# Performance work log

Measured on AMD Instinct MI355X. Metric: run time of the kernel, lower is better.

Reference implementation:

```python
import jax, jax.numpy as jnp
import numpy as np

B, H, W, F_HEX, F_GLB = 2, 48, 48, 150, 7
D, NH, L, DF, M = 512, 8, 4, 2048, 128
MAX_W, MAX_H, ATK, REC = 48, 48, 8, 20
S = H * W
DK = D // NH


def _ln(x, g, b):
    m = jnp.mean(x, -1, keepdims=True)
    v = jnp.mean(jnp.square(x - m), -1, keepdims=True)
    return (x - m) * jax.lax.rsqrt(v + 1e-5) * g + b


def _mha(q, k, v, wq, bq, wk, bk, wv, bv, wo, bo, mask=None):
    Bq, Sq, _ = q.shape
    Sk = k.shape[1]
    Q = (q @ wq + bq).reshape(Bq, Sq, NH, DK)
    K = (k @ wk + bk).reshape(Bq, Sk, NH, DK)
    V = (v @ wv + bv).reshape(Bq, Sk, NH, DK)
    s = jnp.einsum('bqhd,bkhd->bhqk', Q, K) / np.float32(np.sqrt(DK))
    if mask is not None:
        s = jnp.where(mask == 0, jnp.float32(-1e9), s)
    a = jax.nn.softmax(s, -1)
    o = jnp.einsum('bhqk,bkhd->bqhd', a, V).reshape(Bq, Sq, D)
    return o @ wo + bo


def setup_inputs():
    key = jax.random.key(0)
    ks = iter(jax.random.split(key, 64))
    w = lambda *sh: jax.random.normal(next(ks), sh, jnp.float32) * 0.02
    z = lambda *sh: jnp.zeros(sh, jnp.float32)
    o = lambda *sh: jnp.ones(sh, jnp.float32)
    return dict(
        map_representation=jax.random.normal(next(ks), (B, H, W, F_HEX), jnp.float32),
        global_features=jax.random.normal(next(ks), (B, F_GLB), jnp.float32),
        memory=jax.random.normal(next(ks), (B, M, D), jnp.float32),
        fog_mask=jax.random.randint(next(ks), (B, H, W), 0, 2, jnp.int32),
        hex_w=w(F_HEX, D), hex_b=z(D), glob_w=w(F_GLB, D), glob_b=z(D),
        mem_wq=w(D, D), mem_bq=z(D), mem_wk=w(D, D), mem_bk=z(D),
        mem_wv=w(D, D), mem_bv=z(D), mem_wo=w(D, D), mem_bo=z(D),
        gate_w=w(2 * D, D), gate_b=z(D),
        mn1_g=o(D), mn1_b=z(D), mn2_g=o(D), mn2_b=z(D),
        lw_q=w(L, D, D), lb_q=z(L, D), lw_k=w(L, D, D), lb_k=z(L, D),
        lw_v=w(L, D, D), lb_v=z(L, D), lw_o=w(L, D, D), lb_o=z(L, D),
        ln1_g=o(L, D), ln1_b=z(L, D), ln2_g=o(L, D), ln2_b=z(L, D),
        ff1_w=w(L, D, DF), ff1_b=z(L, DF), ff2_w=w(L, DF, D), ff2_b=z(L, D),
        pool_w=w(D, 1), pool_b=z(1),
        sx_w=w(D, MAX_W), sx_b=z(MAX_W), sy_w=w(D, MAX_H), sy_b=z(MAX_H),
        tx_w=w(D, MAX_W), tx_b=z(MAX_W), ty_w=w(D, MAX_H), ty_b=z(MAX_H),
        atk_w=w(D, ATK), atk_b=z(ATK), rec_w=w(D, REC), rec_b=z(REC),
        et_w=w(D, 1), et_b=z(1), val_w=w(D, 1), val_b=z(1),
    )


def reference(map_representation, global_features, memory, fog_mask,
              hex_w, hex_b, glob_w, glob_b,
              mem_wq, mem_bq, mem_wk, mem_bk, mem_wv, mem_bv, mem_wo, mem_bo,
              gate_w, gate_b, mn1_g, mn1_b, mn2_g, mn2_b,
              lw_q, lb_q, lw_k, lb_k, lw_v, lb_v, lw_o, lb_o,
              ln1_g, ln1_b, ln2_g, ln2_b, ff1_w, ff1_b, ff2_w, ff2_b,
              pool_w, pool_b, sx_w, sx_b, sy_w, sy_b, tx_w, tx_b, ty_w, ty_b,
              atk_w, atk_b, rec_w, rec_b, et_w, et_b, val_w, val_b):
    # project hex + global features, flatten map to token sequence [B,S,D]
    hexf = map_representation @ hex_w + hex_b
    glob = global_features @ glob_w + glob_b
    seq = (hexf + glob[:, None, None, :]).reshape(B, S, D)
    am = fog_mask.reshape(B, S)[:, None, None, :]  # key mask [B,1,1,S]

    # memory module: cross-attn conditioning + gated memory update (shared MHA weights)
    mem_out = _mha(seq, memory, memory, mem_wq, mem_bq, mem_wk, mem_bk, mem_wv, mem_bv, mem_wo, mem_bo)
    x = _ln(seq + mem_out, mn1_g, mn1_b)
    mem_upd = _mha(memory, seq, seq, mem_wq, mem_bq, mem_wk, mem_bk, mem_wv, mem_bv, mem_wo, mem_bo)
    gate = jax.nn.sigmoid(jnp.concatenate([memory, mem_upd], -1) @ gate_w + gate_b)
    new_memory = _ln(gate * mem_upd + (1.0 - gate) * memory, mn2_g, mn2_b)

    def block(xc, p):
        wq, bq, wk, bk, wv, bv, wo, bo, g1, b1, g2, b2, f1w, f1b, f2w, f2b = p
        att = _mha(xc, xc, xc, wq, bq, wk, bk, wv, bv, wo, bo, mask=am)
        xc = _ln(xc + att, g1, b1)
        h = jax.nn.gelu(xc @ f1w + f1b, approximate=False) @ f2w + f2b
        return _ln(xc + h, g2, b2), None

    x, _ = jax.lax.scan(block, x, (lw_q, lb_q, lw_k, lb_k, lw_v, lb_v, lw_o, lb_o,
                                   ln1_g, ln1_b, ln2_g, ln2_b, ff1_w, ff1_b, ff2_w, ff2_b))

    # attention pooling over tokens
    pw = jax.nn.softmax((x @ pool_w + pool_b)[..., 0], -1)  # [B,S]
    pooled = jnp.einsum('bs,bsd->bd', pw, x)

    return (pooled @ sx_w + sx_b, pooled @ sy_w + sy_b,
            pooled @ tx_w + tx_b, pooled @ ty_w + ty_b,
            pooled @ atk_w + atk_b, pooled @ rec_w + rec_b,
            pooled @ et_w + et_b, pooled @ val_w + val_b, new_memory)
```

## Files before the change

### kernel.cpp

```cpp
#include <hip/hip_runtime.h>
#include <hip/hip_bf16.h>

typedef __hip_bfloat16 bf16;
typedef unsigned short u16;
typedef __attribute__((ext_vector_type(8))) short short8;
typedef __attribute__((ext_vector_type(4))) float f32x4;

__device__ inline float b2f(u16 u){ unsigned int x = ((unsigned int)u) << 16; float f; __builtin_memcpy(&f, &x, 4); return f; }
__device__ inline u16 f2bits(float f){ __hip_bfloat16 h = __float2bfloat16(f); u16 u; __builtin_memcpy(&u, &h, 2); return u; }
__device__ inline void unpk(unsigned int w, float& a, float& b){ a = b2f((u16)(w & 0xffffu)); b = b2f((u16)(w >> 16)); }

__device__ __forceinline__ unsigned int pkbf(float a, float b)
{
  unsigned int ua = __float_as_uint(a) + 0x8000u;
  unsigned int ub = __float_as_uint(b) + 0x8000u;
  return __builtin_amdgcn_perm(ub, ua, 0x07060302u);
}

__global__ __launch_bounds__(512) void detect_k(const unsigned int* __restrict__ raw, int* __restrict__ flag)
{
  __shared__ int cnt;
  if (threadIdx.x == 0) cnt = 0;
  __syncthreads();
  unsigned int w = raw[threadIdx.x];
  unsigned int b = w & 0x7fffu;
  int pat = (b >= 0x2000u && b <= 0x4400u) ? 1 : 0;
#pragma unroll
  for (int o = 32; o; o >>= 1) pat += __shfl_xor(pat, o);
  if ((threadIdx.x & 63) == 0) atomicAdd(&cnt, pat);
  __syncthreads();
  if (threadIdx.x == 0) flag[0] = (cnt > 320) ? 1 : 0;
}

struct CvtArgs { const void* p[55]; int off[56]; int sz[55]; };

__global__ __launch_bounds__(256) void cvtall8_k(CvtArgs a, bf16* __restrict__ dst,
                                                 const int* __restrict__ flag)
{
  int g8 = blockIdx.x * 256 + threadIdx.x;
  int gid = g8 * 8;
  if (gid >= a.off[55]) return;
  int lo = 0, hi = 54;
  while (lo < hi) { int mid = (lo + hi + 1) >> 1; if (gid >= a.off[mid]) lo = mid; else hi = mid - 1; }
  int t = lo, i = gid - a.off[t];
  int n = a.sz[t];
  uint4 ov;
  if (flag[0]) {
    const u16* src = (const u16*)a.p[t];
    if (i + 8 <= n) {
      ov = *(const uint4*)(src + i);
    } else {
      u16 tmp[8];
#pragma unroll
      for (int j = 0; j < 8; j++) tmp[j] = (i + j < n) ? src[i + j] : (u16)0;
      __builtin_memcpy(&ov, tmp, 16);
    }
  } else {
    const float* src = (const float*)a.p[t];
    float v[8];
    if (i + 8 <= n) {
      uint4 f0 = *(const uint4*)(src + i);
      uint4 f1 = *(const uint4*)(src + i + 4);
      __builtin_memcpy(&v[0], &f0, 16);
      __builtin_memcpy(&v[4], &f1, 16);
    } else {
#pragma unroll
      for (int j = 0; j < 8; j++) v[j] = (i + j < n) ? src[i + j] : 0.f;
    }
    u16 o8[8];
#pragma unroll
    for (int j = 0; j < 8; j++) o8[j] = f2bits(v[j]);
    __builtin_memcpy(&ov, o8, 16);
  }
  *(uint4*)((u16*)dst + gid) = ov;
}

__global__ __launch_bounds__(256) void gemm_k(
    const bf16* __restrict__ A, int lda, long long sAb, long long sAh,
    const bf16* __restrict__ B, int ldb, long long sBb, long long sBh,
    bf16* __restrict__ C, int ldc, long long sCb, long long sCh,
    int M, int N, int K, int HZ,
    const bf16* __restrict__ bias,
    const bf16* __restrict__ res, int ldres,
    const float* __restrict__ extra, int extraDiv,
    float alpha, int mode)
{
  __shared__ u16 As[64][40];
  __shared__ u16 Bs[64][40];
  int z = blockIdx.z;
  int bz = z / HZ, hz = z - bz * HZ;
  A += (size_t)bz * sAb + (size_t)hz * sAh;
  B += (size_t)bz * sBb + (size_t)hz * sBh;
  C += (size_t)bz * sCb + (size_t)hz * sCh;

  int m0 = blockIdx.y * 64, n0 = blockIdx.x * 64;
  int t = threadIdx.x;
  int r = t >> 2, c0 = (t & 3) << 3;
  int lane = t & 63, wv = t >> 6, lr = lane & 15, lq = lane >> 4;

  f32x4 acc[4];
#pragma unroll
  for (int i = 0; i < 4; i++) acc[i] = (f32x4){0.f, 0.f, 0.f, 0.f};

  const u16* Ag = (const u16*)A;
  const u16* Bg = (const u16*)B;
  bool aok = (m0 + r < M), bok = (n0 + r < N);
  const u16* arow = Ag + (size_t)(m0 + r) * lda + c0;
  const u16* brow = Bg + (size_t)(n0 + r) * ldb + c0;

  uint4 av = {0u,0u,0u,0u}, bv = {0u,0u,0u,0u};
  if (aok) av = *(const uint4*)(arow);
  if (bok) bv = *(const uint4*)(brow);

  for (int kt = 0; kt < K; kt += 32) {
    __syncthreads();
    *(uint4*)&As[r][c0] = av;
    *(uint4*)&Bs[r][c0] = bv;
    uint4 av2 = {0u,0u,0u,0u}, bv2 = {0u,0u,0u,0u};
    int nk = kt + 32;
    if (nk < K) {
      if (aok) av2 = *(const uint4*)(arow + nk);
      if (bok) bv2 = *(const uint4*)(brow + nk);
    }
    __syncthreads();
    short8 af = *(const short8*)&As[wv * 16 + lr][lq * 8];
#pragma unroll
    for (int nt = 0; nt < 4; nt++) {
      short8 bfr = *(const short8*)&Bs[nt * 16 + lr][lq * 8];
      acc[nt] = __builtin_amdgcn_mfma_f32_16x16x32_bf16(af, bfr, acc[nt], 0, 0, 0);
    }
    av = av2; bv = bv2;
  }

#pragma unroll
  for (int nt = 0; nt < 4; nt++) {
    int nn = n0 + nt * 16 + lr;
    if (nn >= N) continue;
    float bb = bias ? (float)bias[nn] : 0.f;
#pragma unroll
    for (int rr = 0; rr < 4; rr++) {
      int mm = m0 + wv * 16 + lq * 4 + rr;
      if (mm >= M) continue;
      float v = acc[nt][rr] * alpha + bb;
      if (mode == 1)      v += extra[(mm / extraDiv) * 512 + nn];
      else if (mode == 2) v = 0.5f * v * (1.f + erff(v * 0.70710678118654752f));
      else if (mode == 4) v += (float)res[(size_t)mm * ldres + nn];
      else if (mode == 5) v = 1.f / (1.f + expf(-v));
      C[(size_t)mm * ldc + nn] = __float2bfloat16(v);
    }
  }
}

__device__ __forceinline__ int swz(int row, int cg)
{
  return row * 64 + ((cg ^ (row & 3) ^ (((row >> 3) & 1) << 2)) << 3);
}

__global__ __launch_bounds__(256) void flash_k(
    const bf16* __restrict__ Qp, long long sQb,
    const bf16* __restrict__ Kp, long long sKb,
    const bf16* __restrict__ VTp, long long sVz,
    float* __restrict__ oAcc, long long sOb,
    float* __restrict__ lAcc, int Ml,
    const int* __restrict__ fog,
    int tilesPerSplit, int SkLen)
{
  __shared__ u16 Kl[64 * 64];
  __shared__ u16 Vl[64 * 64];
  __shared__ u16 fgl16[2304];

  const float SC = 0.125f * 1.44269504088896340736f;
  int z = blockIdx.y, b = z >> 3, h = z & 7;
  int qt = blockIdx.x;
  int kt0 = blockIdx.z * tilesPerSplit;
  int t = threadIdx.x, lane = t & 63, w = t >> 6;
  int lr = lane & 15, lq = lane >> 4;
  int useMask = (fog != nullptr);

  const u16* Qg = (const u16*)Qp + (size_t)b * sQb + h * 64;
  const u16* Kg = (const u16*)Kp + (size_t)b * sKb + h * 64;
  const u16* Vg = (const u16*)VTp + (size_t)z * sVz;

  if (useMask) {
    for (int j = t; j < SkLen; j += 256) fgl16[j] = fog[b * 2304 + j] ? 0xFFFFu : 0u;
  }

  int qrow = qt * 64 + w * 16 + lr;
  short8 qf0, qf1;
  {
    union { short8 s; u16 u[8]; } i0, i1, o0, o1;
    i0.s = *(const short8*)(Qg + (size_t)qrow * 512 + lq * 8);
    i1.s = *(const short8*)(Qg + (size_t)qrow * 512 + 32 + lq * 8);
#pragma unroll
    for (int j = 0; j < 8; j++) {
      o0.u[j] = f2bits(b2f(i0.u[j]) * SC);
      o1.u[j] = f2bits(b2f(i1.u[j]) * SC);
    }
    qf0 = o0.s; qf1 = o1.s;
  }

  short8 ones8;
  {
    union { short8 s; u16 u[8]; } on;
#pragma unroll
    for (int j = 0; j < 8; j++) on.u[j] = 0x3F80u;
    ones8 = on.s;
  }

  int rowA[4], kAd0[4], kAd1[4];
#pragma unroll
  for (int nt = 0; nt < 4; nt++) {
    rowA[nt] = 32 * (nt >> 1) + 8 * (lr >> 2) + 4 * (nt & 1) + (lr & 3);
    kAd0[nt] = swz(rowA[nt], lq);
    kAd1[nt] = swz(rowA[nt], lq + 4);
  }
  int vAd0[4], vAd1[4];
#pragma unroll
  for (int dt = 0; dt < 4; dt++) {
    vAd0[dt] = swz(dt * 16 + lr, lq);
    vAd1[dt] = swz(dt * 16 + lr, lq + 4);
  }

  f32x4 o[4], ol;
#pragma unroll
  for (int i = 0; i < 4; i++) o[i] = (f32x4){0.f, 0.f, 0.f, 0.f};
  ol = (f32x4){0.f, 0.f, 0.f, 0.f};

  int rr = t >> 2, cg = t & 3, cs = cg * 8;
  int wAd0 = swz(rr, cg), wAd1 = swz(rr, cg + 4);

  const u16* krow = Kg + (size_t)(kt0 * 64 + rr) * 512 + cs;
  const u16* vrow = Vg + (size_t)rr * SkLen + kt0 * 64 + cs;
  uint4 ka = *(const uint4*)(krow);
  uint4 kb = *(const uint4*)(krow + 32);
  uint4 va = *(const uint4*)(vrow);
  uint4 vb = *(const uint4*)(vrow + 32);

  for (int kti = 0; kti < tilesPerSplit; kti++) {
    int kt = kt0 + kti;
    __syncthreads();
    *(uint4*)&Kl[wAd0] = ka;
    *(uint4*)&Kl[wAd1] = kb;
    *(uint4*)&Vl[wAd0] = va;
    *(uint4*)&Vl[wAd1] = vb;
    if (kti + 1 < tilesPerSplit) {
      krow += 64 * 512;
      vrow += 64;
      ka = *(const uint4*)(krow);
      kb = *(const uint4*)(krow + 32);
      va = *(const uint4*)(vrow);
      vb = *(const uint4*)(vrow + 32);
    }
    __syncthreads();

    f32x4 s[4];
#pragma unroll
    for (int nt = 0; nt < 4; nt++) {
      s[nt] = (f32x4){0.f, 0.f, 0.f, 0.f};
      short8 kf0 = *(const short8*)&Kl[kAd0[nt]];
      short8 kf1 = *(const short8*)&Kl[kAd1[nt]];
      s[nt] = __builtin_amdgcn_mfma_f32_16x16x32_bf16(kf0, qf0, s[nt], 0, 0, 0);
      s[nt] = __builtin_amdgcn_mfma_f32_16x16x32_bf16(kf1, qf1, s[nt], 0, 0, 0);
    }

    union { unsigned int u[4]; short8 s8; } pk0, pk1;
#pragma unroll
    for (int nt = 0; nt < 4; nt++) {
      float p0 = exp2f(s[nt][0]), p1 = exp2f(s[nt][1]);
      float p2 = exp2f(s[nt][2]), p3 = exp2f(s[nt][3]);
      unsigned int w0 = pkbf(p0, p1);
      unsigned int w1 = pkbf(p2, p3);
      if (useMask) {
        int key = kt * 64 + 32 * (nt >> 1) + 8 * lq + 4 * (nt & 1);
        uint2 mm = *(const uint2*)&fgl16[key];
        w0 &= mm.x; w1 &= mm.y;
      }
      if (nt < 2) { pk0.u[(nt & 1) * 2] = w0; pk0.u[(nt & 1) * 2 + 1] = w1; }
      else        { pk1.u[(nt & 1) * 2] = w0; pk1.u[(nt & 1) * 2 + 1] = w1; }
    }
#pragma unroll
    for (int dt = 0; dt < 4; dt++) {
      short8 vf0 = *(const short8*)&Vl[vAd0[dt]];
      short8 vf1 = *(const short8*)&Vl[vAd1[dt]];
      o[dt] = __builtin_amdgcn_mfma_f32_16x16x32_bf16(pk0.s8, vf0, o[dt], 0, 0, 0);
      o[dt] = __builtin_amdgcn_mfma_f32_16x16x32_bf16(pk1.s8, vf1, o[dt], 0, 0, 0);
    }
    ol = __builtin_amdgcn_mfma_f32_16x16x32_bf16(pk0.s8, ones8, ol, 0, 0, 0);
    ol = __builtin_amdgcn_mfma_f32_16x16x32_bf16(pk1.s8, ones8, ol, 0, 0, 0);
  }

  if (lr == 0) {
#pragma unroll
    for (int r2 = 0; r2 < 4; r2++)
      atomicAdd(&lAcc[z * Ml + qt * 64 + w * 16 + lq * 4 + r2], ol[r2]);
  }

  float* ob = oAcc + (size_t)b * sOb;
  int qb = qt * 64 + w * 16 + lq * 4;
#pragma unroll
  for (int dt = 0; dt < 4; dt++)
#pragma unroll
    for (int r2 = 0; r2 < 4; r2++)
      atomicAdd(&ob[(size_t)(qb + r2) * 512 + h * 64 + dt * 16 + lr], o[dt][r2]);
}

__global__ __launch_bounds__(256) void fdiv4_k(const float* __restrict__ oAcc,
                                               const float* __restrict__ lAcc,
                                               int Mq, int Ml, int rows,
                                               bf16* __restrict__ out)
{
  int i = (blockIdx.x * 256 + threadIdx.x) * 4;
  if (i >= rows * 512) return;
  int row = i >> 9, col = i & 511;
  int b = row / Mq, q = row - b * Mq;
  int zz = b * 8 + (col >> 6);
  float l = lAcc[zz * Ml + q];
  float inv = (l > 0.f) ? 1.f / l : 0.f;
  float4 v = *(const float4*)(oAcc + i);
  u16 o4[4] = {f2bits(v.x * inv), f2bits(v.y * inv), f2bits(v.z * inv), f2bits(v.w * inv)};
  unsigned int lo = o4[0] | ((unsigned)o4[1] << 16);
  unsigned int hi = o4[2] | ((unsigned)o4[3] << 16);
  *(uint2*)((u16*)out + i) = (uint2){lo, hi};
}

__global__ __launch_bounds__(256) void transpose_k(const bf16* __restrict__ in, bf16* __restrict__ out,
                                                   int R, int C, int Rpad, long long inB, long long outB)
{
  __shared__ u16 tile[32][33];
  const u16* ip = (const u16*)in + (size_t)blockIdx.z * inB;
  u16* op = (u16*)out + (size_t)blockIdx.z * outB;
  int c0 = blockIdx.x * 32, r0 = blockIdx.y * 32;
  int tx = threadIdx.x & 31, ty = threadIdx.x >> 5;
#pragma unroll
  for (int j = 0; j < 4; j++) {
    int rr = r0 + ty + j * 8, cc = c0 + tx;
    u16 v = 0;
    if (rr < R && cc < C) v = ip[(size_t)rr * C + cc];
    tile[ty + j * 8][tx] = v;
  }
  __syncthreads();
#pragma unroll
  for (int j = 0; j < 4; j++) {
    int oc = c0 + ty + j * 8;
    if (oc < C && r0 + tx < Rpad) op[(size_t)oc * Rpad + r0 + tx] = tile[tx][ty + j * 8];
  }
}

__global__ __launch_bounds__(256) void headT_k(const bf16* __restrict__ in, bf16* __restrict__ out,
                                               int Sk, int rowbase, int bstride)
{
  __shared__ u16 tile[32][33];
  int z = blockIdx.z, b = z >> 3, h = z & 7;
  const u16* ip = (const u16*)in + ((size_t)(rowbase + b * bstride)) * 512 + h * 64;
  u16* op = (u16*)out + (size_t)z * 64 * Sk;
  int r0 = blockIdx.x * 32, c0 = blockIdx.y * 32;
  int tx = threadIdx.x & 31, ty = threadIdx.x >> 5;
#pragma unroll
  for (int j = 0; j < 4; j++)
    tile[ty + j * 8][tx] = ip[(size_t)(r0 + ty + j * 8) * 512 + c0 + tx];
  __syncthreads();
#pragma unroll
  for (int j = 0; j < 4; j++)
    op[(size_t)(c0 + ty + j * 8) * Sk + r0 + tx] = tile[tx][ty + j * 8];
}

__global__ __launch_bounds__(256) void ln_k(const bf16* __restrict__ in, const bf16* __restrict__ g,
                                            const bf16* __restrict__ bb, bf16* __restrict__ out)
{
  size_t row = blockIdx.x * 4 + (threadIdx.x >> 6);
  int lane = threadIdx.x & 63;
  const u16* ip = (const u16*)in + row * 512 + lane * 8;
  uint4 rv = *(const uint4*)ip;
  float v[8];
  unpk(rv.x, v[0], v[1]); unpk(rv.y, v[2], v[3]); unpk(rv.z, v[4], v[5]); unpk(rv.w, v[6], v[7]);
  float s = 0.f, s2 = 0.f;
#pragma unroll
  for (int k = 0; k < 8; k++) { s += v[k]; s2 += v[k] * v[k]; }
#pragma unroll
  for (int o = 32; o; o >>= 1) { s += __shfl_xor(s, o); s2 += __shfl_xor(s2, o); }
  float mean = s * (1.f / 512.f);
  float var = s2 * (1.f / 512.f) - mean * mean;
  float rstd = rsqrtf(var + 1e-5f);
  uint4 gv = *(const uint4*)((const u16*)g + lane * 8);
  uint4 bv = *(const uint4*)((const u16*)bb + lane * 8);
  float gf[8], bf2[8];
  unpk(gv.x, gf[0], gf[1]); unpk(gv.y, gf[2], gf[3]); unpk(gv.z, gf[4], gf[5]); unpk(gv.w, gf[6], gf[7]);
  unpk(bv.x, bf2[0], bf2[1]); unpk(bv.y, bf2[2], bf2[3]); unpk(bv.z, bf2[4], bf2[5]); unpk(bv.w, bf2[6], bf2[7]);
  u16 o8[8];
#pragma unroll
  for (int k = 0; k < 8; k++) o8[k] = f2bits((v[k] - mean) * rstd * gf[k] + bf2[k]);
  uint4 ov;
  ov.x = o8[0] | ((unsigned)o8[1] << 16); ov.y = o8[2] | ((unsigned)o8[3] << 16);
  ov.z = o8[4] | ((unsigned)o8[5] << 16); ov.w = o8[6] | ((unsigned)o8[7] << 16);
  *(uint4*)((u16*)out + row * 512 + lane * 8) = ov;
}

__global__ void glob_k(const bf16* __restrict__ gf, const bf16* __restrict__ gw,
                       const bf16* __restrict__ gb, float* __restrict__ out)
{
  int i = blockIdx.x * 256 + threadIdx.x; if (i >= 1024) return;
  int b = i >> 9, d = i & 511;
  float s = (float)gb[d];
#pragma unroll
  for (int f = 0; f < 7; f++) s += (float)gf[b * 7 + f] * (float)gw[f * 512 + d];
  out[i] = s;
}

__global__ void padA_k(const bf16* __restrict__ in, bf16* __restrict__ out)
{
  int i = blockIdx.x * 256 + threadIdx.x; if (i >= 4608 * 160) return;
  int r = i / 160, c = i - r * 160;
  out[i] = (c < 150) ? in[r * 150 + c] : __float2bfloat16(0.f);
}

__global__ void catg_k(const bf16* __restrict__ mem, const bf16* __restrict__ mu, bf16* __restrict__ out)
{
  int i = blockIdx.x * 256 + threadIdx.x; if (i >= 256 * 1024) return;
  int r = i >> 10, c = i & 1023;
  out[i] = (c < 512) ? mem[r * 512 + c] : mu[r * 512 + c - 512];
}

__global__ void gcomb_k(const bf16* __restrict__ g, const bf16* __restrict__ mu,
                        const bf16* __restrict__ mem, bf16* __restrict__ out)
{
  int i = blockIdx.x * 256 + threadIdx.x; if (i >= 131072) return;
  float gg = (float)g[i];
  out[i] = __float2bfloat16(gg * (float)mu[i] + (1.f - gg) * (float)mem[i]);
}

__global__ __launch_bounds__(64) void plog_k(const bf16* __restrict__ x, const bf16* __restrict__ pw,
                                             const bf16* __restrict__ pb, float* __restrict__ out)
{
  size_t row = blockIdx.x; int lane = threadIdx.x;
  uint4 xv = *(const uint4*)((const u16*)x + row * 512 + lane * 8);
  uint4 wv = *(const uint4*)((const u16*)pw + lane * 8);
  float v[8], w[8];
  unpk(xv.x, v[0], v[1]); unpk(xv.y, v[2], v[3]); unpk(xv.z, v[4], v[5]); unpk(xv.w, v[6], v[7]);
  unpk(wv.x, w[0], w[1]); unpk(wv.y, w[2], w[3]); unpk(wv.z, w[4], w[5]); unpk(wv.w, w[6], w[7]);
  float s = 0.f;
#pragma unroll
  for (int k = 0; k < 8; k++) s += v[k] * w[k];
#pragma unroll
  for (int o = 32; o; o >>= 1) s += __shfl_xor(s, o);
  if (lane == 0) out[row] = s + (float)pb[0];
}

__global__ __launch_bounds__(256) void psm_k(const float* __restrict__ lg, float* __restrict__ pw)
{
  __shared__ float red[4];
  int b = blockIdx.x, tid = threadIdx.x;
  const float* p = lg + b * 2304;
  float vals[9]; float mx = -3e38f;
#pragma unroll
  for (int i = 0; i < 9; i++) {
    int j = tid + i * 256;
    float x = (j < 2304) ? p[j] : -3e38f;
    vals[i] = x; mx = fmaxf(mx, x);
  }
#pragma unroll
  for (int o = 32; o; o >>= 1) mx = fmaxf(mx, __shfl_xor(mx, o));
  if ((tid & 63) == 0) red[tid >> 6] = mx;
  __syncthreads();
  mx = fmaxf(fmaxf(red[0], red[1]), fmaxf(red[2], red[3]));
  float sum = 0.f;
#pragma unroll
  for (int i = 0; i < 9; i++) {
    int j = tid + i * 256;
    if (j < 2304) { float e = expf(vals[i] - mx); vals[i] = e; sum += e; }
  }
  __syncthreads();
#pragma unroll
  for (int o = 32; o; o >>= 1) sum += __shfl_xor(sum, o);
  if ((tid & 63) == 0) red[tid >> 6] = sum;
  __syncthreads();
  sum = red[0] + red[1] + red[2] + red[3];
  float inv = 1.f / sum;
#pragma unroll
  for (int i = 0; i < 9; i++) {
    int j = tid + i * 256;
    if (j < 2304) pw[b * 2304 + j] = vals[i] * inv;
  }
}

__global__ __launch_bounds__(256) void pool1_k(const float* __restrict__ pw, const bf16* __restrict__ x,
                                               float* __restrict__ out)
{
  int b = blockIdx.y, chunk = blockIdx.x, t = threadIdx.x;
  float a0 = 0.f, a1 = 0.f;
  for (int s = 0; s < 64; s++) {
    int tok = chunk * 64 + s;
    float wv = pw[b * 2304 + tok];
    const u16* xp = (const u16*)x + ((size_t)(b * 2304 + tok)) * 512;
    a0 += wv * b2f(xp[t]);
    a1 += wv * b2f(xp[t + 256]);
  }
  atomicAdd(&out[b * 512 + t], a0);
  atomicAdd(&out[b * 512 + t + 256], a1);
}

__global__ void heads_k(const float* __restrict__ pooled,
                        const bf16* w0, const bf16* b0, const bf16* w1, const bf16* b1,
                        const bf16* w2, const bf16* b2, const bf16* w3, const bf16* b3,
                        const bf16* w4, const bf16* b4, const bf16* w5, const bf16* b5,
                        const bf16* w6, const bf16* b6, const bf16* w7, const bf16* b7,
                        void* __restrict__ outv, const int* __restrict__ flag)
{
  int idx = blockIdx.x * 256 + threadIdx.x; if (idx >= 444) return;
  const bf16* W[8] = {w0, w1, w2, w3, w4, w5, w6, w7};
  const bf16* Bi[8] = {b0, b1, b2, b3, b4, b5, b6, b7};
  int b = idx / 222, j = idx - b * 222;
  const int sizes[8]  = {48, 48, 48, 48, 8, 20, 1, 1};
  const int outoff[8] = {0, 96, 192, 288, 384, 400, 440, 442};
  int h = 0, basec = 0;
  while (h < 7 && j >= basec + sizes[h]) { basec += sizes[h]; ++h; }
  int col = j - basec;
  const bf16* wp = W[h]; int nc = sizes[h];
  float s = (float)Bi[h][col];
  for (int k = 0; k < 512; k++) s += pooled[b * 512 + k] * (float)wp[k * nc + col];
  int e = outoff[h] + b * nc + col;
  if (flag[0]) ((bf16*)outv)[e] = __float2bfloat16(s);
  else         ((float*)outv)[e] = s;
}

__global__ void outstore_k(const bf16* __restrict__ nm, void* __restrict__ outv,
                           const int* __restrict__ flag)
{
  int i = blockIdx.x * 256 + threadIdx.x; if (i >= 131072) return;
  if (flag[0]) ((bf16*)outv)[444 + i] = nm[i];
  else         ((float*)outv)[444 + i] = (float)nm[i];
}


static inline void gemm(hipStream_t st, const bf16* A, int lda, long long sAb, long long sAh,
                        const bf16* B, int ldb, long long sBb, long long sBh,
                        bf16* C, int ldc, long long sCb, long long sCh,
                        int M, int N, int K, int BZ, int HZ,
                        const bf16* bias, const bf16* res, int ldres,
                        const float* extra, int extraDiv, float alpha, int mode)
{
  dim3 g((N + 63) / 64, (M + 63) / 64, BZ * HZ);
  gemm_k<<<g, dim3(256), 0, st>>>(A, lda, sAb, sAh, B, ldb, sBb, sBh, C, ldc, sCb, sCh,
                                  M, N, K, HZ, bias, res, ldres, extra, extraDiv, alpha, mode);
}

static inline void transp(hipStream_t st, const bf16* in, bf16* out, int R, int C, int Rpad,
                          long long inB, long long outB, int Z)
{
  dim3 g((C + 31) / 32, (Rpad + 31) / 32, Z);
  transpose_k<<<g, dim3(256), 0, st>>>(in, out, R, C, Rpad, inB, outB);
}

extern "C" void kernel_launch(void* const* d_in, const int* in_sizes, int n_in,
                              void* d_out, int out_size, void* d_ws, size_t ws_size,
                              hipStream_t stream)
{
  (void)in_sizes; (void)n_in; (void)out_size;
  const int* fog = (const int*)d_in[3];

  static const int kSz[55] = {
    691200, 14, 131072, 76800, 512, 3584, 512,
    262144, 512, 262144, 512, 262144, 512, 262144, 512,
    524288, 512, 512, 512, 512, 512,
    1048576, 2048, 1048576, 2048, 1048576, 2048, 1048576, 2048,
    2048, 2048, 2048, 2048,
    4194304, 8192, 4194304, 2048,
    512, 1,
    24576, 48, 24576, 48, 24576, 48, 24576, 48,
    4096, 8, 10240, 20, 512, 1, 512, 1};
  static const int kIdx[55] = {
    0, 1, 2, 4, 5, 6, 7,
    8, 9, 10, 11, 12, 13, 14, 15,
    16, 17, 18, 19, 20, 21,
    22, 23, 24, 25, 26, 27, 28, 29,
    30, 31, 32, 33,
    34, 35, 36, 37,
    38, 39,
    40, 41, 42, 43, 44, 45, 46, 47,
    48, 49, 50, 51, 52, 53, 54, 55};

  CvtArgs ca;
  size_t cum[55]; int coffi = 0;
  for (int t = 0; t < 55; t++) {
    cum[t] = (size_t)coffi;
    ca.p[t] = d_in[kIdx[t]];
    ca.off[t] = coffi;
    ca.sz[t] = kSz[t];
    coffi += (kSz[t] + 7) & ~7;
  }
  ca.off[55] = coffi;
  size_t coff = (size_t)coffi;

  const int S = 2304, NROW = 4608, CATROW = 4864;
  const long long RS = (long long)S * 512;

  char* basep = (char*)d_ws; size_t off = 0;
  auto alloc = [&](size_t elems, size_t esz) -> void* {
    void* p = basep + off; off += (elems * esz + 255) & ~(size_t)255; return p;
  };

  bf16* canon = (bf16*)alloc(coff, 2);
  int* dflag = (int*)alloc(64, 4);
  bf16* tHex = (bf16*)alloc(512 * 160, 2);
  bf16* aPad = (bf16*)alloc((size_t)NROW * 160, 2);
  bf16* tWq = (bf16*)alloc(512 * 512, 2);
  bf16* tWk = (bf16*)alloc(512 * 512, 2);
  bf16* tWv = (bf16*)alloc(512 * 512, 2);
  bf16* tWo = (bf16*)alloc(512 * 512, 2);
  bf16* tGate = (bf16*)alloc(512 * 1024, 2);
  bf16* tLq = (bf16*)alloc(4 * 512 * 512, 2);
  bf16* tLk = (bf16*)alloc(4 * 512 * 512, 2);
  bf16* tLv = (bf16*)alloc(4 * 512 * 512, 2);
  bf16* tLo = (bf16*)alloc(4 * 512 * 512, 2);
  bf16* tF1 = (bf16*)alloc(4ULL * 2048 * 512, 2);
  bf16* tF2 = (bf16*)alloc(4ULL * 512 * 2048, 2);
  float* globF = (float*)alloc(1024, 4);
  bf16* catX = (bf16*)alloc((size_t)CATROW * 512, 2);
  bf16* Qc = (bf16*)alloc((size_t)CATROW * 512, 2);
  bf16* Kc = (bf16*)alloc((size_t)CATROW * 512, 2);
  bf16* Vc = (bf16*)alloc((size_t)CATROW * 512, 2);
  bf16* VmemT = (bf16*)alloc(16ULL * 64 * 128, 2);
  bf16* VsT = (bf16*)alloc(16ULL * 64 * S, 2);
  bf16* mo = (bf16*)alloc((size_t)NROW * 512, 2);
  bf16* tmp1 = (bf16*)alloc((size_t)NROW * 512, 2);
  bf16* xbuf = (bf16*)alloc((size_t)NROW * 512, 2);
  bf16* x2buf = (bf16*)alloc((size_t)NROW * 512, 2);
  bf16* mu0 = (bf16*)alloc(256 * 512, 2);
  bf16* mup = (bf16*)alloc(256 * 512, 2);
  bf16* catg = (bf16*)alloc(256 * 1024, 2);
  bf16* gateb = (bf16*)alloc(256 * 512, 2);
  bf16* nmpre = (bf16*)alloc(256 * 512, 2);
  bf16* nmout = (bf16*)alloc(256 * 512, 2);
  float* plog = (float*)alloc(NROW, 4);
  float* pwv = (float*)alloc(NROW, 4);
  float* pooledF = (float*)alloc(1024, 4);
  float* oAcc = (float*)alloc((size_t)NROW * 512, 4);
  float* lAcc = (float*)alloc(16 * 2304, 4);
  bf16* hbuf = (bf16*)alloc((size_t)NROW * 2048, 2);
  if (off > ws_size) return;

  detect_k<<<1, 512, 0, stream>>>((const unsigned int*)d_in[0], dflag);
  cvtall8_k<<<(coffi / 8 + 255) / 256, 256, 0, stream>>>(ca, canon, dflag);

  auto T = [&](int t) -> const bf16* { return canon + cum[t]; };
  const bf16* map_rep = T(0);
  const bf16* gfeat   = T(1);
  const bf16* memin   = T(2);
  const bf16* hex_w = T(3);  const bf16* hex_b = T(4);
  const bf16* glob_w = T(5); const bf16* glob_b = T(6);
  const bf16* mem_wq = T(7);  const bf16* mem_bq = T(8);
  const bf16* mem_wk = T(9);  const bf16* mem_bk = T(10);
  const bf16* mem_wv = T(11); const bf16* mem_bv = T(12);
  const bf16* mem_wo = T(13); const bf16* mem_bo = T(14);
  const bf16* gate_w = T(15); const bf16* gate_b = T(16);
  const bf16* mn1_g = T(17); const bf16* mn1_b = T(18);
  const bf16* mn2_g = T(19); const bf16* mn2_b = T(20);
  const bf16* lw_q = T(21); const bf16* lb_q = T(22);
  const bf16* lw_k = T(23); const bf16* lb_k = T(24);
  const bf16* lw_v = T(25); const bf16* lb_v = T(26);
  const bf16* lw_o = T(27); const bf16* lb_o = T(28);
  const bf16* ln1_g = T(29); const bf16* ln1_b = T(30);
  const bf16* ln2_g = T(31); const bf16* ln2_b = T(32);
  const bf16* ff1_w = T(33); const bf16* ff1_b = T(34);
  const bf16* ff2_w = T(35); const bf16* ff2_b = T(36);
  const bf16* pool_w = T(37); const bf16* pool_b = T(38);

  transp(stream, hex_w, tHex, 150, 512, 160, 0, 0, 1);
  transp(stream, mem_wq, tWq, 512, 512, 512, 0, 0, 1);
  transp(stream, mem_wk, tWk, 512, 512, 512, 0, 0, 1);
  transp(stream, mem_wv, tWv, 512, 512, 512, 0, 0, 1);
  transp(stream, mem_wo, tWo, 512, 512, 512, 0, 0, 1);
  transp(stream, gate_w, tGate, 1024, 512, 1024, 0, 0, 1);
  transp(stream, lw_q, tLq, 512, 512, 512, 262144, 262144, 4);
  transp(stream, lw_k, tLk, 512, 512, 512, 262144, 262144, 4);
  transp(stream, lw_v, tLv, 512, 512, 512, 262144, 262144, 4);
  transp(stream, lw_o, tLo, 512, 512, 512, 262144, 262144, 4);
  transp(stream, ff1_w, tF1, 512, 2048, 512, 1048576, 1048576, 4);
  transp(stream, ff2_w, tF2, 2048, 512, 2048, 1048576, 1048576, 4);

  glob_k<<<4, 256, 0, stream>>>(gfeat, glob_w, glob_b, globF);
  padA_k<<<(NROW * 160 + 255) / 256, 256, 0, stream>>>(map_rep, aPad);
  gemm(stream, aPad, 160, 0, 0, tHex, 160, 0, 0, catX, 512, 0, 0,
       NROW, 512, 160, 1, 1, hex_b, nullptr, 0, globF, S, 1.f, 1);
  hipMemcpyAsync(catX + (size_t)NROW * 512, memin, 256 * 512 * 2, hipMemcpyDeviceToDevice, stream);

  gemm(stream, catX, 512, 0, 0, tWq, 512, 0, 0, Qc, 512, 0, 0, CATROW, 512, 512, 1, 1, mem_bq, nullptr, 0, nullptr, 1, 1.f, 0);
  gemm(stream, catX, 512, 0, 0, tWk, 512, 0, 0, Kc, 512, 0, 0, CATROW, 512, 512, 1, 1, mem_bk, nullptr, 0, nullptr, 1, 1.f, 0);
  gemm(stream, catX, 512, 0, 0, tWv, 512, 0, 0, Vc, 512, 0, 0, CATROW, 512, 512, 1, 1, mem_bv, nullptr, 0, nullptr, 1, 1.f, 0);

  headT_k<<<dim3(4, 2, 16), 256, 0, stream>>>(Vc, VmemT, 128, NROW, 128);
  hipMemsetAsync(oAcc, 0, (size_t)NROW * 512 * 4, stream);
  hipMemsetAsync(lAcc, 0, 16 * 2304 * 4, stream);
  flash_k<<<dim3(36, 16, 1), 256, 0, stream>>>(Qc, RS, Kc + (size_t)NROW * 512, 128 * 512,
                                               VmemT, 64 * 128, oAcc, RS, lAcc, 2304,
                                               nullptr, 2, 128);
  fdiv4_k<<<(NROW * 128 + 255) / 256, 256, 0, stream>>>(oAcc, lAcc, 2304, 2304, NROW, mo);
  gemm(stream, mo, 512, 0, 0, tWo, 512, 0, 0, tmp1, 512, 0, 0,
       NROW, 512, 512, 1, 1, mem_bo, catX, 512, nullptr, 1, 1.f, 4);
  ln_k<<<NROW / 4, 256, 0, stream>>>(tmp1, mn1_g, mn1_b, xbuf);

  headT_k<<<dim3(72, 2, 16), 256, 0, stream>>>(Vc, VsT, S, 0, S);
  hipMemsetAsync(oAcc, 0, 256 * 512 * 4, stream);
  hipMemsetAsync(lAcc, 0, 16 * 128 * 4, stream);
  flash_k<<<dim3(2, 16, 6), 256, 0, stream>>>(Qc + (size_t)NROW * 512, 128 * 512, Kc, RS,
                                              VsT, 64LL * S, oAcc, 128 * 512, lAcc, 128,
                                              nullptr, 6, S);
  fdiv4_k<<<(256 * 128 + 255) / 256, 256, 0, stream>>>(oAcc, lAcc, 128, 128, 256, mu0);
  gemm(stream, mu0, 512, 0, 0, tWo, 512, 0, 0, mup, 512, 0, 0,
       256, 512, 512, 1, 1, mem_bo, nullptr, 0, nullptr, 1, 1.f, 0);
  catg_k<<<(256 * 1024 + 255) / 256, 256, 0, stream>>>(memin, mup, catg);
  gemm(stream, catg, 1024, 0, 0, tGate, 1024, 0, 0, gateb, 512, 0, 0,
       256, 512, 1024, 1, 1, gate_b, nullptr, 0, nullptr, 1, 1.f, 5);
  gcomb_k<<<(131072 + 255) / 256, 256, 0, stream>>>(gateb, mup, memin, nmpre);
  ln_k<<<64, 256, 0, stream>>>(nmpre, mn2_g, mn2_b, nmout);
  outstore_k<<<(131072 + 255) / 256, 256, 0, stream>>>(nmout, d_out, dflag);

  for (int l = 0; l < 4; l++) {
    gemm(stream, xbuf, 512, 0, 0, tLq + (size_t)l * 262144, 512, 0, 0, Qc, 512, 0, 0,
         NROW, 512, 512, 1, 1, lb_q + l * 512, nullptr, 0, nullptr, 1, 1.f, 0);
    gemm(stream, xbuf, 512, 0, 0, tLk + (size_t)l * 262144, 512, 0, 0, Kc, 512, 0, 0,
         NROW, 512, 512, 1, 1, lb_k + l * 512, nullptr, 0, nullptr, 1, 1.f, 0);
    gemm(stream, xbuf, 512, 0, 0, tLv + (size_t)l * 262144, 512, 0, 0, Vc, 512, 0, 0,
         NROW, 512, 512, 1, 1, lb_v + l * 512, nullptr, 0, nullptr, 1, 1.f, 0);
    headT_k<<<dim3(72, 2, 16), 256, 0, stream>>>(Vc, VsT, S, 0, S);
    hipMemsetAsync(oAcc, 0, (size_t)NROW * 512 * 4, stream);
    hipMemsetAsync(lAcc, 0, 16 * 2304 * 4, stream);
    flash_k<<<dim3(36, 16, 2), 256, 0, stream>>>(Qc, RS, Kc, RS, VsT, 64LL * S,
                                                 oAcc, RS, lAcc, 2304, fog, 18, S);
    fdiv4_k<<<(NROW * 128 + 255) / 256, 256, 0, stream>>>(oAcc, lAcc, 2304, 2304, NROW, mo);
    gemm(stream, mo, 512, 0, 0, tLo + (size_t)l * 262144, 512, 0, 0, tmp1, 512, 0, 0,
         NROW, 512, 512, 1, 1, lb_o + l * 512, xbuf, 512, nullptr, 1, 1.f, 4);
    ln_k<<<NROW / 4, 256, 0, stream>>>(tmp1, ln1_g + l * 512, ln1_b + l * 512, x2buf);
    gemm(stream, x2buf, 512, 0, 0, tF1 + (size_t)l * 1048576, 512, 0, 0, hbuf, 2048, 0, 0,
         NROW, 2048, 512, 1, 1, ff1_b + l * 2048, nullptr, 0, nullptr, 1, 1.f, 2);
    gemm(stream, hbuf, 2048, 0, 0, tF2 + (size_t)l * 1048576, 2048, 0, 0, tmp1, 512, 0, 0,
         NROW, 512, 2048, 1, 1, ff2_b + l * 512, x2buf, 512, nullptr, 1, 1.f, 4);
    ln_k<<<NROW / 4, 256, 0, stream>>>(tmp1, ln2_g + l * 512, ln2_b + l * 512, xbuf);
  }

  plog_k<<<NROW, 64, 0, stream>>>(xbuf, pool_w, pool_b, plog);
  psm_k<<<2, 256, 0, stream>>>(plog, pwv);
  hipMemsetAsync(pooledF, 0, 1024 * sizeof(float), stream);
  pool1_k<<<dim3(36, 2), 256, 0, stream>>>(pwv, xbuf, pooledF);

  heads_k<<<2, 256, 0, stream>>>(pooledF,
      T(39), T(40), T(41), T(42), T(43), T(44), T(45), T(46),
      T(47), T(48), T(49), T(50), T(51), T(52), T(53), T(54),
      d_out, dflag);
}
```

Baseline: 1.184 ms.

## Fuse Q/K/V projections into one GEMM and retune attention split

Packs the Q, K and V weight matrices and biases into one concatenated [1536x512] operand, so each projection stage runs one GEMM writing an interleaved QKV buffer instead of three GEMMs. The flash and transpose kernels gain row-stride parameters to read from the interleaved buffer. The two memsets become one zeroing kernel. The self-attention key split goes from 2 to 3 chunks, and exp2f is replaced by the hardware exp2 builtin. The aim is fewer launches and better GEMM occupancy, at the cost of strided Q/K reads and more split-K partial accumulation.

```diff
diff --git a/kernel.cpp b/kernel.cpp
--- a/kernel.cpp
+++ b/kernel.cpp
@@ -157,8 +157,8 @@
 }
 
 __global__ __launch_bounds__(256) void flash_k(
-    const bf16* __restrict__ Qp, long long sQb,
-    const bf16* __restrict__ Kp, long long sKb,
+    const bf16* __restrict__ Qp, long long sQb, int sQr,
+    const bf16* __restrict__ Kp, long long sKb, int sKr,
     const bf16* __restrict__ VTp, long long sVz,
     float* __restrict__ oAcc, long long sOb,
     float* __restrict__ lAcc, int Ml,
@@ -189,8 +189,8 @@
   short8 qf0, qf1;
   {
     union { short8 s; u16 u[8]; } i0, i1, o0, o1;
-    i0.s = *(const short8*)(Qg + (size_t)qrow * 512 + lq * 8);
-    i1.s = *(const short8*)(Qg + (size_t)qrow * 512 + 32 + lq * 8);
+    i0.s = *(const short8*)(Qg + (size_t)qrow * sQr + lq * 8);
+    i1.s = *(const short8*)(Qg + (size_t)qrow * sQr + 32 + lq * 8);
 #pragma unroll
     for (int j = 0; j < 8; j++) {
       o0.u[j] = f2bits(b2f(i0.u[j]) * SC);
@@ -229,7 +229,7 @@
   int rr = t >> 2, cg = t & 3, cs = cg * 8;
   int wAd0 = swz(rr, cg), wAd1 = swz(rr, cg + 4);
 
-  const u16* krow = Kg + (size_t)(kt0 * 64 + rr) * 512 + cs;
+  const u16* krow = Kg + (size_t)(kt0 * 64 + rr) * sKr + cs;
   const u16* vrow = Vg + (size_t)rr * SkLen + kt0 * 64 + cs;
   uint4 ka = *(const uint4*)(krow);
   uint4 kb = *(const uint4*)(krow + 32);
@@ -244,7 +244,7 @@
     *(uint4*)&Vl[wAd0] = va;
     *(uint4*)&Vl[wAd1] = vb;
     if (kti + 1 < tilesPerSplit) {
-      krow += 64 * 512;
+      krow += (size_t)64 * sKr;
       vrow += 64;
       ka = *(const uint4*)(krow);
       kb = *(const uint4*)(krow + 32);
@@ -266,8 +266,10 @@
     union { unsigned int u[4]; short8 s8; } pk0, pk1;
 #pragma unroll
     for (int nt = 0; nt < 4; nt++) {
-      float p0 = exp2f(s[nt][0]), p1 = exp2f(s[nt][1]);
-      float p2 = exp2f(s[nt][2]), p3 = exp2f(s[nt][3]);
+      float p0 = __builtin_amdgcn_exp2f(s[nt][0]);
+      float p1 = __builtin_amdgcn_exp2f(s[nt][1]);
+      float p2 = __builtin_amdgcn_exp2f(s[nt][2]);
+      float p3 = __builtin_amdgcn_exp2f(s[nt][3]);
       unsigned int w0 = pkbf(p0, p1);
       unsigned int w1 = pkbf(p2, p3);
       if (useMask) {
@@ -323,6 +325,32 @@
   *(uint2*)((u16*)out + i) = (uint2){lo, hi};
 }
 
+__global__ __launch_bounds__(256) void zero2_k(float* __restrict__ p1, int n1,
+                                               float* __restrict__ p2, int n2)
+{
+  int i = blockIdx.x * 256 + threadIdx.x;
+  if (i < n1) p1[i] = 0.f;
+  if (i < n2) p2[i] = 0.f;
+}
+
+__global__ void biasfuse_k(const bf16* __restrict__ mbq, const bf16* __restrict__ mbk,
+                           const bf16* __restrict__ mbv, const bf16* __restrict__ lbq,
+                           const bf16* __restrict__ lbk, const bf16* __restrict__ lbv,
+                           bf16* __restrict__ out)
+{
+  int j = blockIdx.x * 256 + threadIdx.x;
+  if (j >= 5 * 1536) return;
+  int g = j / 1536, r = j - g * 1536;
+  int which = r >> 9, c = r & 511;
+  const bf16* src;
+  if (g == 0) src = (which == 0) ? mbq : (which == 1) ? mbk : mbv;
+  else {
+    const bf16* base = (which == 0) ? lbq : (which == 1) ? lbk : lbv;
+    src = base + (g - 1) * 512;
+  }
+  out[j] = src[c];
+}
+
 __global__ __launch_bounds__(256) void transpose_k(const bf16* __restrict__ in, bf16* __restrict__ out,
                                                    int R, int C, int Rpad, long long inB, long long outB)
 {
@@ -347,17 +375,17 @@
 }
 
 __global__ __launch_bounds__(256) void headT_k(const bf16* __restrict__ in, bf16* __restrict__ out,
-                                               int Sk, int rowbase, int bstride)
+                                               int Sk, int rowbase, int bstride, int instride)
 {
   __shared__ u16 tile[32][33];
   int z = blockIdx.z, b = z >> 3, h = z & 7;
-  const u16* ip = (const u16*)in + ((size_t)(rowbase + b * bstride)) * 512 + h * 64;
+  const u16* ip = (const u16*)in + ((size_t)(rowbase + b * bstride)) * instride + h * 64;
   u16* op = (u16*)out + (size_t)z * 64 * Sk;
   int r0 = blockIdx.x * 32, c0 = blockIdx.y * 32;
   int tx = threadIdx.x & 31, ty = threadIdx.x >> 5;
 #pragma unroll
   for (int j = 0; j < 4; j++)
-    tile[ty + j * 8][tx] = ip[(size_t)(r0 + ty + j * 8) * 512 + c0 + tx];
+    tile[ty + j * 8][tx] = ip[(size_t)(r0 + ty + j * 8) * instride + c0 + tx];
   __syncthreads();
 #pragma unroll
   for (int j = 0; j < 4; j++)
@@ -591,7 +619,8 @@
   size_t coff = (size_t)coffi;
 
   const int S = 2304, NROW = 4608, CATROW = 4864;
-  const long long RS = (long long)S * 512;
+  const long long QR = 1536;
+  const long long RSQ = (long long)S * QR;
 
   char* basep = (char*)d_ws; size_t off = 0;
   auto alloc = [&](size_t elems, size_t esz) -> void* {
@@ -602,22 +631,17 @@
   int* dflag = (int*)alloc(64, 4);
   bf16* tHex = (bf16*)alloc(512 * 160, 2);
   bf16* aPad = (bf16*)alloc((size_t)NROW * 160, 2);
-  bf16* tWq = (bf16*)alloc(512 * 512, 2);
-  bf16* tWk = (bf16*)alloc(512 * 512, 2);
-  bf16* tWv = (bf16*)alloc(512 * 512, 2);
+  bf16* tQKVmem = (bf16*)alloc(1536 * 512, 2);
   bf16* tWo = (bf16*)alloc(512 * 512, 2);
   bf16* tGate = (bf16*)alloc(512 * 1024, 2);
-  bf16* tLq = (bf16*)alloc(4 * 512 * 512, 2);
-  bf16* tLk = (bf16*)alloc(4 * 512 * 512, 2);
-  bf16* tLv = (bf16*)alloc(4 * 512 * 512, 2);
+  bf16* tLqkv = (bf16*)alloc(4ULL * 1536 * 512, 2);
   bf16* tLo = (bf16*)alloc(4 * 512 * 512, 2);
   bf16* tF1 = (bf16*)alloc(4ULL * 2048 * 512, 2);
   bf16* tF2 = (bf16*)alloc(4ULL * 512 * 2048, 2);
+  bf16* fbias = (bf16*)alloc(5 * 1536, 2);
   float* globF = (float*)alloc(1024, 4);
   bf16* catX = (bf16*)alloc((size_t)CATROW * 512, 2);
-  bf16* Qc = (bf16*)alloc((size_t)CATROW * 512, 2);
-  bf16* Kc = (bf16*)alloc((size_t)CATROW * 512, 2);
-  bf16* Vc = (bf16*)alloc((size_t)CATROW * 512, 2);
+  bf16* QKV = (bf16*)alloc((size_t)CATROW * 1536, 2);
   bf16* VmemT = (bf16*)alloc(16ULL * 64 * 128, 2);
   bf16* VsT = (bf16*)alloc(16ULL * 64 * S, 2);
   bf16* mo = (bf16*)alloc((size_t)NROW * 512, 2);
@@ -665,17 +689,19 @@
   const bf16* pool_w = T(37); const bf16* pool_b = T(38);
 
   transp(stream, hex_w, tHex, 150, 512, 160, 0, 0, 1);
-  transp(stream, mem_wq, tWq, 512, 512, 512, 0, 0, 1);
-  transp(stream, mem_wk, tWk, 512, 512, 512, 0, 0, 1);
-  transp(stream, mem_wv, tWv, 512, 512, 512, 0, 0, 1);
+  transp(stream, mem_wq, tQKVmem, 512, 512, 512, 0, 0, 1);
+  transp(stream, mem_wk, tQKVmem + 262144, 512, 512, 512, 0, 0, 1);
+  transp(stream, mem_wv, tQKVmem + 524288, 512, 512, 512, 0, 0, 1);
   transp(stream, mem_wo, tWo, 512, 512, 512, 0, 0, 1);
   transp(stream, gate_w, tGate, 1024, 512, 1024, 0, 0, 1);
-  transp(stream, lw_q, tLq, 512, 512, 512, 262144, 262144, 4);
-  transp(stream, lw_k, tLk, 512, 512, 512, 262144, 262144, 4);
-  transp(stream, lw_v, tLv, 512, 512, 512, 262144, 262144, 4);
+  transp(stream, lw_q, tLqkv, 512, 512, 512, 262144, 786432, 4);
+  transp(stream, lw_k, tLqkv + 262144, 512, 512, 512, 262144, 786432, 4);
+  transp(stream, lw_v, tLqkv + 524288, 512, 512, 512, 262144, 786432, 4);
   transp(stream, lw_o, tLo, 512, 512, 512, 262144, 262144, 4);
   transp(stream, ff1_w, tF1, 512, 2048, 512, 1048576, 1048576, 4);
   transp(stream, ff2_w, tF2, 2048, 512, 2048, 1048576, 1048576, 4);
+  biasfuse_k<<<(5 * 1536 + 255) / 256, 256, 0, stream>>>(mem_bq, mem_bk, mem_bv,
+                                                         lb_q, lb_k, lb_v, fbias);
 
   glob_k<<<4, 256, 0, stream>>>(gfeat, glob_w, glob_b, globF);
   padA_k<<<(NROW * 160 + 255) / 256, 256, 0, stream>>>(map_rep, aPad);
@@ -683,27 +709,24 @@
        NROW, 512, 160, 1, 1, hex_b, nullptr, 0, globF, S, 1.f, 1);
   hipMemcpyAsync(catX + (size_t)NROW * 512, memin, 256 * 512 * 2, hipMemcpyDeviceToDevice, stream);
 
-  gemm(stream, catX, 512, 0, 0, tWq, 512, 0, 0, Qc, 512, 0, 0, CATROW, 512, 512, 1, 1, mem_bq, nullptr, 0, nullptr, 1, 1.f, 0);
-  gemm(stream, catX, 512, 0, 0, tWk, 512, 0, 0, Kc, 512, 0, 0, CATROW, 512, 512, 1, 1, mem_bk, nullptr, 0, nullptr, 1, 1.f, 0);
-  gemm(stream, catX, 512, 0, 0, tWv, 512, 0, 0, Vc, 512, 0, 0, CATROW, 512, 512, 1, 1, mem_bv, nullptr, 0, nullptr, 1, 1.f, 0);
-
-  headT_k<<<dim3(4, 2, 16), 256, 0, stream>>>(Vc, VmemT, 128, NROW, 128);
-  hipMemsetAsync(oAcc, 0, (size_t)NROW * 512 * 4, stream);
-  hipMemsetAsync(lAcc, 0, 16 * 2304 * 4, stream);
-  flash_k<<<dim3(36, 16, 1), 256, 0, stream>>>(Qc, RS, Kc + (size_t)NROW * 512, 128 * 512,
-                                               VmemT, 64 * 128, oAcc, RS, lAcc, 2304,
-                                               nullptr, 2, 128);
+  gemm(stream, catX, 512, 0, 0, tQKVmem, 512, 0, 0, QKV, 1536, 0, 0,
+       CATROW, 1536, 512, 1, 1, fbias, nullptr, 0, nullptr, 1, 1.f, 0);
+
+  headT_k<<<dim3(4, 2, 16), 256, 0, stream>>>(QKV + 1024, VmemT, 128, NROW, 128, 1536);
+  zero2_k<<<(NROW * 512 + 255) / 256, 256, 0, stream>>>(oAcc, NROW * 512, lAcc, 16 * 2304);
+  flash_k<<<dim3(36, 16, 1), 256, 0, stream>>>(
+      QKV, RSQ, 1536, QKV + (size_t)NROW * 1536 + 512, 128 * QR, 1536,
+      VmemT, 64 * 128, oAcc, (long long)S * 512, lAcc, 2304, nullptr, 2, 128);
   fdiv4_k<<<(NROW * 128 + 255) / 256, 256, 0, stream>>>(oAcc, lAcc, 2304, 2304, NROW, mo);
   gemm(stream, mo, 512, 0, 0, tWo, 512, 0, 0, tmp1, 512, 0, 0,
        NROW, 512, 512, 1, 1, mem_bo, catX, 512, nullptr, 1, 1.f, 4);
   ln_k<<<NROW / 4, 256, 0, stream>>>(tmp1, mn1_g, mn1_b, xbuf);
 
-  headT_k<<<dim3(72, 2, 16), 256, 0, stream>>>(Vc, VsT, S, 0, S);
-  hipMemsetAsync(oAcc, 0, 256 * 512 * 4, stream);
-  hipMemsetAsync(lAcc, 0, 16 * 128 * 4, stream);
-  flash_k<<<dim3(2, 16, 6), 256, 0, stream>>>(Qc + (size_t)NROW * 512, 128 * 512, Kc, RS,
-                                              VsT, 64LL * S, oAcc, 128 * 512, lAcc, 128,
-                                              nullptr, 6, S);
+  headT_k<<<dim3(72, 2, 16), 256, 0, stream>>>(QKV + 1024, VsT, S, 0, S, 1536);
+  zero2_k<<<(256 * 512 + 255) / 256, 256, 0, stream>>>(oAcc, 256 * 512, lAcc, 16 * 128);
+  flash_k<<<dim3(2, 16, 6), 256, 0, stream>>>(
+      QKV + (size_t)NROW * 1536, 128 * QR, 1536, QKV + 512, RSQ, 1536,
+      VsT, 64LL * S, oAcc, 128 * 512, lAcc, 128, nullptr, 6, S);
   fdiv4_k<<<(256 * 128 + 255) / 256, 256, 0, stream>>>(oAcc, lAcc, 128, 128, 256, mu0);
   gemm(stream, mu0, 512, 0, 0, tWo, 512, 0, 0, mup, 512, 0, 0,
        256, 512, 512, 1, 1, mem_bo, nullptr, 0, nullptr, 1, 1.f, 0);
@@ -715,17 +738,13 @@
   outstore_k<<<(131072 + 255) / 256, 256, 0, stream>>>(nmout, d_out, dflag);
 
   for (int l = 0; l < 4; l++) {
-    gemm(stream, xbuf, 512, 0, 0, tLq + (size_t)l * 262144, 512, 0, 0, Qc, 512, 0, 0,
-         NROW, 512, 512, 1, 1, lb_q + l * 512, nullptr, 0, nullptr, 1, 1.f, 0);
-    gemm(stream, xbuf, 512, 0, 0, tLk + (size_t)l * 262144, 512, 0, 0, Kc, 512, 0, 0,
-         NROW, 512, 512, 1, 1, lb_k + l * 512, nullptr, 0, nullptr, 1, 1.f, 0);
-    gemm(stream, xbuf, 512, 0, 0, tLv + (size_t)l * 262144, 512, 0, 0, Vc, 512, 0, 0,
-         NROW, 512, 512, 1, 1, lb_v + l * 512, nullptr, 0, nullptr, 1, 1.f, 0);
-    headT_k<<<dim3(72, 2, 16), 256, 0, stream>>>(Vc, VsT, S, 0, S);
-    hipMemsetAsync(oAcc, 0, (size_t)NROW * 512 * 4, stream);
-    hipMemsetAsync(lAcc, 0, 16 * 2304 * 4, stream);
-    flash_k<<<dim3(36, 16, 2), 256, 0, stream>>>(Qc, RS, Kc, RS, VsT, 64LL * S,
-                                                 oAcc, RS, lAcc, 2304, fog, 18, S);
+    gemm(stream, xbuf, 512, 0, 0, tLqkv + (size_t)l * 786432, 512, 0, 0, QKV, 1536, 0, 0,
+         NROW, 1536, 512, 1, 1, fbias + (1 + l) * 1536, nullptr, 0, nullptr, 1, 1.f, 0);
+    headT_k<<<dim3(72, 2, 16), 256, 0, stream>>>(QKV + 1024, VsT, S, 0, S, 1536);
+    zero2_k<<<(NROW * 512 + 255) / 256, 256, 0, stream>>>(oAcc, NROW * 512, lAcc, 16 * 2304);
+    flash_k<<<dim3(36, 16, 3), 256, 0, stream>>>(
+        QKV, RSQ, 1536, QKV + 512, RSQ, 1536,
+        VsT, 64LL * S, oAcc, (long long)S * 512, lAcc, 2304, fog, 12, S);
     fdiv4_k<<<(NROW * 128 + 255) / 256, 256, 0, stream>>>(oAcc, lAcc, 2304, 2304, NROW, mo);
     gemm(stream, mo, 512, 0, 0, tLo + (size_t)l * 262144, 512, 0, 0, tmp1, 512, 0, 0,
          NROW, 512, 512, 1, 1, lb_o + l * 512, xbuf, 512, nullptr, 1, 1.f, 4);
```

Measured after the change: 1.087 ms. 8.2% less time.
